# Performance work log

Hardware: AMD Instinct MI355X
Metric: run time of the kernel (lower is better)

The kernel has to match this reference:

```python
import jax, jax.numpy as jnp
import numpy as np

KS = 31  # kernel size
PAD = KS // 2

def _dw_conv_plus_sum(x, w, C):
    # depthwise conv (groups=C, same padding) + global spatial-sum bias
    x_sum = jnp.sum(x, axis=(-2, -1), keepdims=True)
    y = jax.lax.conv_general_dilated(
        x, w,
        window_strides=(1, 1),
        padding=((PAD, PAD), (PAD, PAD)),
        dimension_numbers=('NCHW', 'OIHW', 'NCHW'),
        feature_group_count=C)
    return y + x_sum

def setup_inputs() -> dict:
    key = jax.random.key(0)
    k1, k2 = jax.random.split(key)
    bs, C, H, W = 16, 192, 64, 64
    qkv = jax.random.normal(k1, (bs, 3 * C, H * W), dtype=jnp.float32)
    weights = jax.random.normal(k2, (C, 1, KS, KS), dtype=jnp.float32) * 0.01
    return {"qkv": qkv, "weights": weights, "H": H, "W": W}

def reference(qkv, weights, H, W):
    bs, ch3, _ = qkv.shape
    C = ch3 // 3
    dtype = qkv.dtype
    x = qkv.reshape(bs, ch3, H, W).astype(jnp.float32)
    q, k, v = jnp.split(x, 3, axis=1)  # each (bs, C, H, W)
    # softmax over flattened spatial dims
    k = jax.nn.softmax(k.reshape(bs, C, H * W), axis=-1).reshape(bs, C, H, W)
    kv = k * v
    w = jnp.expm1(weights.astype(jnp.float32))  # (C,1,KS,KS)
    k_c = _dw_conv_plus_sum(k, w, C)
    kv_c = _dw_conv_plus_sum(kv, w, C)
    out = jax.nn.sigmoid(q) * kv_c / (k_c + 1e-8)
    return out.reshape(bs, C, H * W).astype(dtype)
```

## Files before the change

### kernel.cpp

```cpp
#include <hip/hip_runtime.h>
#include <math.h>


#define C_     192
#define HW_    4096
#define KS_    31
#define IROWS_ 94
#define ISTR_  100
#define WCOLS_ 96
#define NT_    128

typedef _Float16 f16;
typedef _Float16 f16x4 __attribute__((ext_vector_type(4)));
typedef _Float16 f16x8 __attribute__((ext_vector_type(8)));
typedef float    f32x16 __attribute__((ext_vector_type(16)));

__device__ __forceinline__ void conv_pass(const f16* __restrict__ img,
                                          const unsigned int* __restrict__ wp,
                                          int lane, int ybase,
                                          f32x16* acc0, f32x16* acc1)
{
    const int l5  = lane >> 5;
    const int l31 = lane & 31;
    int aoff = (ybase + l31) * ISTR_ + 4 * l5;
    const unsigned int* bp0 = wp + (32 + 4 * l5 - l31);
#pragma unroll 1
    for (int dy = 0; dy < KS_; ++dy) {
        f16x8 A[6];
        const f16* ap = img + aoff;
#pragma unroll
        for (int cc = 0; cc < 6; ++cc) {
            f16x4 lo = *(const f16x4*)(ap + cc * 16);
            f16x4 hi = *(const f16x4*)(ap + cc * 16 + 8);
            A[cc] = __builtin_shufflevector(lo, hi, 0, 1, 2, 3, 4, 5, 6, 7);
        }
        const unsigned int* bp = bp0 + dy * WCOLS_;
#pragma unroll
        for (int kc = 0; kc < 4; ++kc) {
            uint4 bw;
            bw.x = bp[kc * 16 + 0];
            bw.y = bp[kc * 16 + 2];
            bw.z = bp[kc * 16 + 8];
            bw.w = bp[kc * 16 + 10];
            f16x8 B = __builtin_bit_cast(f16x8, bw);
            *acc0 = __builtin_amdgcn_mfma_f32_32x32x16_f16(A[kc],     B, *acc0, 0, 0, 0);
            *acc1 = __builtin_amdgcn_mfma_f32_32x32x16_f16(A[kc + 2], B, *acc1, 0, 0, 0);
        }
        aoff += ISTR_;
    }
}

__global__ __launch_bounds__(NT_, 2)
void aft_mfma(const float* __restrict__ qkv,
              const float* __restrict__ wts,
              float* __restrict__ out)
{
    __shared__ __align__(16) f16 IMG[IROWS_ * ISTR_];
    __shared__ unsigned int WP[KS_ * WCOLS_];
    __shared__ float red[8];

    const int bc = blockIdx.x;
    const int b  = bc / C_;
    const int c  = bc - b * C_;
    const float* qrow = qkv + ((size_t)b * (3 * C_) + c) * HW_;
    const float* krow = qrow + (size_t)C_ * HW_;
    const float* vrow = qrow + (size_t)(2 * C_) * HW_;
    float*       orow = out + ((size_t)b * C_ + c) * HW_;

    const int t = threadIdx.x, lane = t & 63, wid = t >> 6;

    unsigned int* IMGu = (unsigned int*)IMG;
    for (int i = t; i < (IROWS_ * ISTR_) / 2; i += NT_) IMGu[i] = 0u;
    const float* wch = wts + (size_t)c * (KS_ * KS_);
    for (int i = t; i < KS_ * WCOLS_; i += NT_) {
        const int dy = i / WCOLS_, cw = i - dy * WCOLS_;
        const int d0 = cw - 33, d1 = cw - 32;
        const float w0 = (d0 >= 0 && d0 < KS_) ? expm1f(wch[dy * KS_ + d0]) : 0.f;
        const float w1 = (d1 >= 0 && d1 < KS_) ? expm1f(wch[dy * KS_ + d1]) : 0.f;
        union { unsigned int u; f16 h[2]; } pk;
        pk.h[0] = (f16)w0; pk.h[1] = (f16)w1;
        WP[i] = pk.u;
    }

    float kvv[32];
    float pm = -3.0e38f;
#pragma unroll
    for (int i = 0; i < 8; ++i) {
        float4 v = ((const float4*)krow)[t + NT_ * i];
        kvv[4*i+0] = v.x; kvv[4*i+1] = v.y; kvv[4*i+2] = v.z; kvv[4*i+3] = v.w;
        pm = fmaxf(pm, fmaxf(fmaxf(v.x, v.y), fmaxf(v.z, v.w)));
    }
#pragma unroll
    for (int s = 32; s; s >>= 1) pm = fmaxf(pm, __shfl_xor(pm, s));
    if (lane == 0) red[wid] = pm;
    __syncthreads();
    const float m = fmaxf(red[0], red[1]);

    const int ry = t >> 4;
    const int rx = (t & 15) * 4;
    float ps = 0.f;
#pragma unroll
    for (int i = 0; i < 8; ++i) {
        f16x4 h;
#pragma unroll
        for (int e = 0; e < 4; ++e) {
            float ev = __expf(kvv[4*i+e] - m);
            ps += ev;
            h[e] = (f16)ev;
        }
        *(f16x4*)(&IMG[(ry + 8 * i + 15) * ISTR_ + rx + 16]) = h;
    }
#pragma unroll
    for (int s = 32; s; s >>= 1) ps += __shfl_xor(ps, s);
    if (lane == 0) red[2 + wid] = ps;
    __syncthreads();
    const float Z = red[2] + red[3];

    f32x16 accA0, accA1;
#pragma unroll
    for (int r = 0; r < 16; ++r) { accA0[r] = 0.f; accA1[r] = 0.f; }
    conv_pass(IMG, WP, lane, 32 * wid, &accA0, &accA1);
    __syncthreads();

    float skv = 0.f;
#pragma unroll
    for (int i = 0; i < 8; ++i) {
        float4 v = ((const float4*)vrow)[t + NT_ * i];
        f16* pp = &IMG[(ry + 8 * i + 15) * ISTR_ + rx + 16];
        f16x4 h = *(f16x4*)pp;
        float a0 = (float)h[0] * v.x;
        float a1 = (float)h[1] * v.y;
        float a2 = (float)h[2] * v.z;
        float a3 = (float)h[3] * v.w;
        skv += (a0 + a1) + (a2 + a3);
        h[0] = (f16)a0; h[1] = (f16)a1; h[2] = (f16)a2; h[3] = (f16)a3;
        *(f16x4*)pp = h;
    }
#pragma unroll
    for (int s = 32; s; s >>= 1) skv += __shfl_xor(skv, s);
    if (lane == 0) red[4 + wid] = skv;
    __syncthreads();
    const float sumkv = red[4] + red[5];

    f32x16 accB0, accB1;
#pragma unroll
    for (int r = 0; r < 16; ++r) { accB0[r] = 0.f; accB1[r] = 0.f; }
    conv_pass(IMG, WP, lane, 32 * wid, &accB0, &accB1);

    const float l5f = (float)0; (void)l5f;
    const int yb = 32 * wid + 4 * (lane >> 5);
    const int l31 = lane & 31;
#pragma unroll
    for (int tt = 0; tt < 2; ++tt) {
        const f32x16& ka = tt ? accA1 : accA0;
        const f32x16& va = tt ? accB1 : accB0;
        const int x = 32 * tt + l31;
#pragma unroll
        for (int r = 0; r < 16; ++r) {
            const int y = yb + (r & 3) + 8 * (r >> 2);
            const int idx = y * 64 + x;
            const float qv = qrow[idx];
            const float den = (ka[r] + Z + Z * 1e-8f) * (1.f + __expf(-qv));
            orow[idx] = (va[r] + sumkv) * __builtin_amdgcn_rcpf(den);
        }
    }
}

extern "C" void kernel_launch(void* const* d_in, const int* in_sizes, int n_in,
                              void* d_out, int out_size, void* d_ws, size_t ws_size,
                              hipStream_t stream)
{
    const float* qkv = (const float*)d_in[0];
    const float* wts = (const float*)d_in[1];
    float* out       = (float*)d_out;
    (void)in_sizes; (void)n_in; (void)d_ws; (void)ws_size; (void)out_size;

    aft_mfma<<<dim3(16 * C_), dim3(NT_), 0, stream>>>(qkv, wts, out);
}
```

Measured before the change: 299.5 us.

## Fuse both conv passes, precompute weight fragments in workspace, reorder blocks by channel

A separate kernel now builds the per-channel expm1 weight fragments in MFMA B-operand layout in global workspace, so each block no longer recomputes expm1 weights into shared memory. The main kernel keeps both the softmax-exp image and the k*v image in shared memory and runs the two convolutions in one dy loop, sharing B loads, which it prefetches one row ahead. Blocks are ordered channel-major so neighbouring blocks reuse the same weight fragments from cache. The image layout is swizzled for 16-byte loads. This roughly doubles shared memory per block and adds a kernel launch, with a fallback path when workspace is missing.

```diff
diff --git a/kernel.cpp b/kernel.cpp
--- a/kernel.cpp
+++ b/kernel.cpp
@@ -3,26 +3,176 @@
 
 
 #define C_     192
+#define BS_    16
 #define HW_    4096
 #define KS_    31
+#define NT_    128
+
 #define IROWS_ 94
-#define ISTR_  100
-#define WCOLS_ 96
-#define NT_    128
+#define ISTR_  104
+#define IMGSZ_ (IROWS_ * ISTR_)
+#define NFRAG_ 160
+#define BF_PER_C_ (KS_ * NFRAG_ * 8)
+#define BF_BYTES_ ((size_t)C_ * BF_PER_C_ * 2)
 
 typedef _Float16 f16;
 typedef _Float16 f16x4 __attribute__((ext_vector_type(4)));
 typedef _Float16 f16x8 __attribute__((ext_vector_type(8)));
 typedef float    f32x16 __attribute__((ext_vector_type(16)));
 
-__device__ __forceinline__ void conv_pass(const f16* __restrict__ img,
-                                          const unsigned int* __restrict__ wp,
-                                          int lane, int ybase,
-                                          f32x16* acc0, f32x16* acc1)
+__global__ __launch_bounds__(256)
+void build_bfrags(const float* __restrict__ wts, f16* __restrict__ bf)
+{
+    const int fi = blockIdx.x * 256 + threadIdx.x;
+    if (fi >= C_ * KS_ * NFRAG_) return;
+    const int s81 = fi % 80;
+    int rest = fi / 80;
+    const int l5 = rest & 1; rest >>= 1;
+    const int dy = rest % KS_;
+    const int c  = rest / KS_;
+    const float* wrow = wts + (size_t)c * (KS_ * KS_) + dy * KS_;
+    const int s = s81 - 31;
+    f16x8 o;
+#pragma unroll
+    for (int j = 0; j < 8; ++j) {
+        const int tap = s + 4 * l5 + (j & 3) + 8 * (j >> 2) - 1;
+        o[j] = (tap >= 0 && tap < KS_) ? (f16)expm1f(wrow[tap]) : (f16)0.f;
+    }
+    *reinterpret_cast<f16x8*>(bf + (size_t)fi * 8) = o;
+}
+
+__global__ __launch_bounds__(NT_, 2)
+void aft_mfma2(const float* __restrict__ qkv,
+               const f16* __restrict__ bf,
+               float* __restrict__ out)
+{
+    __shared__ __align__(16) f16 IMG[2 * IMGSZ_];
+    __shared__ float red[8];
+
+    const int blk = blockIdx.x;
+    const int c = blk >> 4;
+    const int b = blk & 15;
+    const float* qrow = qkv + ((size_t)b * (3 * C_) + c) * HW_;
+    const float* krow = qrow + (size_t)C_ * HW_;
+    const float* vrow = qrow + (size_t)(2 * C_) * HW_;
+    float*       orow = out + ((size_t)b * C_ + c) * HW_;
+
+    const int t = threadIdx.x, lane = t & 63, wid = t >> 6;
+    const int l5 = lane >> 5, l31 = lane & 31;
+
+    uint4* I4 = reinterpret_cast<uint4*>(IMG);
+    for (int i = t; i < (2 * IMGSZ_) / 8; i += NT_) I4[i] = make_uint4(0u, 0u, 0u, 0u);
+
+    float pm = -3.0e38f;
+#pragma unroll
+    for (int i = 0; i < 8; ++i) {
+        float4 k4 = ((const float4*)krow)[t + NT_ * i];
+        pm = fmaxf(pm, fmaxf(fmaxf(k4.x, k4.y), fmaxf(k4.z, k4.w)));
+    }
+#pragma unroll
+    for (int s = 32; s; s >>= 1) pm = fmaxf(pm, __shfl_xor(pm, s));
+    if (lane == 0) red[wid] = pm;
+    __syncthreads();
+    const float m = fmaxf(red[0], red[1]);
+
+    const int ry  = t >> 4;
+    const int rx4 = t & 15;
+    const int g   = 1 + (rx4 >> 2);
+    const int q   = rx4 & 3;
+    const int qp  = (q == 1) ? 2 : (q == 2) ? 1 : q;
+    float zs = 0.f, skv = 0.f;
+#pragma unroll
+    for (int i = 0; i < 8; ++i) {
+        float4 k4 = ((const float4*)krow)[t + NT_ * i];
+        float4 v4 = ((const float4*)vrow)[t + NT_ * i];
+        float e0 = __expf(k4.x - m), e1 = __expf(k4.y - m);
+        float e2 = __expf(k4.z - m), e3 = __expf(k4.w - m);
+        zs += (e0 + e1) + (e2 + e3);
+        float a0 = e0 * v4.x, a1 = e1 * v4.y, a2 = e2 * v4.z, a3 = e3 * v4.w;
+        skv += (a0 + a1) + (a2 + a3);
+        const int row = ry + 8 * i + 15;
+        f16* pE = (f16*)((char*)IMG + row * (ISTR_ * 2) + g * 32 + qp * 8);
+        f16x4 he; he[0] = (f16)e0; he[1] = (f16)e1; he[2] = (f16)e2; he[3] = (f16)e3;
+        f16x4 hk; hk[0] = (f16)a0; hk[1] = (f16)a1; hk[2] = (f16)a2; hk[3] = (f16)a3;
+        *reinterpret_cast<f16x4*>(pE) = he;
+        *reinterpret_cast<f16x4*>(pE + IMGSZ_) = hk;
+    }
+#pragma unroll
+    for (int s = 32; s; s >>= 1) { zs += __shfl_xor(zs, s); skv += __shfl_xor(skv, s); }
+    if (lane == 0) { red[2 + wid] = zs; red[4 + wid] = skv; }
+    __syncthreads();
+    const float Z     = red[2] + red[3];
+    const float sumkv = red[4] + red[5];
+
+    f32x16 aE0, aE1, aK0, aK1;
+#pragma unroll
+    for (int r = 0; r < 16; ++r) { aE0[r] = 0.f; aE1[r] = 0.f; aK0[r] = 0.f; aK1[r] = 0.f; }
+
+    const f16* bl = bf + (size_t)c * BF_PER_C_ + l5 * 640 + (31 - l31) * 8;
+    int abyte = ((32 * wid) + l31) * (ISTR_ * 2) + l5 * 16;
+
+    f16x8 Bc[4];
+#pragma unroll
+    for (int kc = 0; kc < 4; ++kc)
+        Bc[kc] = *reinterpret_cast<const f16x8*>(bl + kc * 128);
+
+#pragma unroll 1
+    for (int dy = 0; dy < KS_; ++dy) {
+        const int dyn = (dy + 1 < KS_) ? dy + 1 : dy;
+        const f16* bln = bl + dyn * (NFRAG_ * 8);
+        f16x8 Bn[4];
+#pragma unroll
+        for (int kc = 0; kc < 4; ++kc)
+            Bn[kc] = *reinterpret_cast<const f16x8*>(bln + kc * 128);
+
+        f16x8 AE[6], AK[6];
+        const char* ap = (const char*)IMG + abyte;
+#pragma unroll
+        for (int cc = 0; cc < 6; ++cc) {
+            AE[cc] = *reinterpret_cast<const f16x8*>(ap + cc * 32);
+            AK[cc] = *reinterpret_cast<const f16x8*>(ap + cc * 32 + IMGSZ_ * 2);
+        }
+#pragma unroll
+        for (int kc = 0; kc < 4; ++kc) {
+            aE0 = __builtin_amdgcn_mfma_f32_32x32x16_f16(AE[kc],     Bc[kc], aE0, 0, 0, 0);
+            aE1 = __builtin_amdgcn_mfma_f32_32x32x16_f16(AE[kc + 2], Bc[kc], aE1, 0, 0, 0);
+            aK0 = __builtin_amdgcn_mfma_f32_32x32x16_f16(AK[kc],     Bc[kc], aK0, 0, 0, 0);
+            aK1 = __builtin_amdgcn_mfma_f32_32x32x16_f16(AK[kc + 2], Bc[kc], aK1, 0, 0, 0);
+        }
+#pragma unroll
+        for (int kc = 0; kc < 4; ++kc) Bc[kc] = Bn[kc];
+        abyte += ISTR_ * 2;
+    }
+
+    const int yb = 32 * wid + 4 * l5;
+#pragma unroll
+    for (int tt = 0; tt < 2; ++tt) {
+        const f32x16& ke = tt ? aE1 : aE0;
+        const f32x16& kv = tt ? aK1 : aK0;
+        const int x = 32 * tt + l31;
+#pragma unroll
+        for (int r = 0; r < 16; ++r) {
+            const int y = yb + (r & 3) + 8 * (r >> 2);
+            const int idx = y * 64 + x;
+            const float qv = qrow[idx];
+            const float den = (ke[r] + Z + Z * 1e-8f) * (1.f + __expf(-qv));
+            orow[idx] = (kv[r] + sumkv) * __builtin_amdgcn_rcpf(den);
+        }
+    }
+}
+
+#define FB_IROWS_ 94
+#define FB_ISTR_  100
+#define FB_WCOLS_ 96
+
+__device__ __forceinline__ void conv_pass_fb(const f16* __restrict__ img,
+                                             const unsigned int* __restrict__ wp,
+                                             int lane, int ybase,
+                                             f32x16* acc0, f32x16* acc1)
 {
     const int l5  = lane >> 5;
     const int l31 = lane & 31;
-    int aoff = (ybase + l31) * ISTR_ + 4 * l5;
+    int aoff = (ybase + l31) * FB_ISTR_ + 4 * l5;
     const unsigned int* bp0 = wp + (32 + 4 * l5 - l31);
 #pragma unroll 1
     for (int dy = 0; dy < KS_; ++dy) {
@@ -34,7 +184,7 @@
             f16x4 hi = *(const f16x4*)(ap + cc * 16 + 8);
             A[cc] = __builtin_shufflevector(lo, hi, 0, 1, 2, 3, 4, 5, 6, 7);
         }
-        const unsigned int* bp = bp0 + dy * WCOLS_;
+        const unsigned int* bp = bp0 + dy * FB_WCOLS_;
 #pragma unroll
         for (int kc = 0; kc < 4; ++kc) {
             uint4 bw;
@@ -46,7 +196,7 @@
             *acc0 = __builtin_amdgcn_mfma_f32_32x32x16_f16(A[kc],     B, *acc0, 0, 0, 0);
             *acc1 = __builtin_amdgcn_mfma_f32_32x32x16_f16(A[kc + 2], B, *acc1, 0, 0, 0);
         }
-        aoff += ISTR_;
+        aoff += FB_ISTR_;
     }
 }
 
@@ -55,8 +205,8 @@
               const float* __restrict__ wts,
               float* __restrict__ out)
 {
-    __shared__ __align__(16) f16 IMG[IROWS_ * ISTR_];
-    __shared__ unsigned int WP[KS_ * WCOLS_];
+    __shared__ __align__(16) f16 IMGF[FB_IROWS_ * FB_ISTR_];
+    __shared__ unsigned int WP[KS_ * FB_WCOLS_];
     __shared__ float red[8];
 
     const int bc = blockIdx.x;
@@ -69,11 +219,11 @@
 
     const int t = threadIdx.x, lane = t & 63, wid = t >> 6;
 
-    unsigned int* IMGu = (unsigned int*)IMG;
-    for (int i = t; i < (IROWS_ * ISTR_) / 2; i += NT_) IMGu[i] = 0u;
+    unsigned int* IMGu = (unsigned int*)IMGF;
+    for (int i = t; i < (FB_IROWS_ * FB_ISTR_) / 2; i += NT_) IMGu[i] = 0u;
     const float* wch = wts + (size_t)c * (KS_ * KS_);
-    for (int i = t; i < KS_ * WCOLS_; i += NT_) {
-        const int dy = i / WCOLS_, cw = i - dy * WCOLS_;
+    for (int i = t; i < KS_ * FB_WCOLS_; i += NT_) {
+        const int dy = i / FB_WCOLS_, cw = i - dy * FB_WCOLS_;
         const int d0 = cw - 33, d1 = cw - 32;
         const float w0 = (d0 >= 0 && d0 < KS_) ? expm1f(wch[dy * KS_ + d0]) : 0.f;
         const float w1 = (d1 >= 0 && d1 < KS_) ? expm1f(wch[dy * KS_ + d1]) : 0.f;
@@ -108,7 +258,7 @@
             ps += ev;
             h[e] = (f16)ev;
         }
-        *(f16x4*)(&IMG[(ry + 8 * i + 15) * ISTR_ + rx + 16]) = h;
+        *(f16x4*)(&IMGF[(ry + 8 * i + 15) * FB_ISTR_ + rx + 16]) = h;
     }
 #pragma unroll
     for (int s = 32; s; s >>= 1) ps += __shfl_xor(ps, s);
@@ -119,14 +269,14 @@
     f32x16 accA0, accA1;
 #pragma unroll
     for (int r = 0; r < 16; ++r) { accA0[r] = 0.f; accA1[r] = 0.f; }
-    conv_pass(IMG, WP, lane, 32 * wid, &accA0, &accA1);
+    conv_pass_fb(IMGF, WP, lane, 32 * wid, &accA0, &accA1);
     __syncthreads();
 
     float skv = 0.f;
 #pragma unroll
     for (int i = 0; i < 8; ++i) {
         float4 v = ((const float4*)vrow)[t + NT_ * i];
-        f16* pp = &IMG[(ry + 8 * i + 15) * ISTR_ + rx + 16];
+        f16* pp = &IMGF[(ry + 8 * i + 15) * FB_ISTR_ + rx + 16];
         f16x4 h = *(f16x4*)pp;
         float a0 = (float)h[0] * v.x;
         float a1 = (float)h[1] * v.y;
@@ -145,9 +295,8 @@
     f32x16 accB0, accB1;
 #pragma unroll
     for (int r = 0; r < 16; ++r) { accB0[r] = 0.f; accB1[r] = 0.f; }
-    conv_pass(IMG, WP, lane, 32 * wid, &accB0, &accB1);
-
-    const float l5f = (float)0; (void)l5f;
+    conv_pass_fb(IMGF, WP, lane, 32 * wid, &accB0, &accB1);
+
     const int yb = 32 * wid + 4 * (lane >> 5);
     const int l31 = lane & 31;
 #pragma unroll
@@ -173,7 +322,14 @@
     const float* qkv = (const float*)d_in[0];
     const float* wts = (const float*)d_in[1];
     float* out       = (float*)d_out;
-    (void)in_sizes; (void)n_in; (void)d_ws; (void)ws_size; (void)out_size;
-
-    aft_mfma<<<dim3(16 * C_), dim3(NT_), 0, stream>>>(qkv, wts, out);
-}
+    (void)in_sizes; (void)n_in; (void)out_size;
+
+    if (ws_size >= BF_BYTES_ && d_ws != nullptr) {
+        f16* bfr = (f16*)d_ws;
+        const int total = C_ * KS_ * NFRAG_;
+        build_bfrags<<<dim3((total + 255) / 256), dim3(256), 0, stream>>>(wts, bfr);
+        aft_mfma2<<<dim3(BS_ * C_), dim3(NT_), 0, stream>>>(qkv, bfr, out);
+    } else {
+        aft_mfma<<<dim3(BS_ * C_), dim3(NT_), 0, stream>>>(qkv, wts, out);
+    }
+}
```

Result: slower. 308.3 us (+2.9%).
